# Kernel tuning notes

Measured on AMD Instinct MI355X. Metric: run time of the kernel, lower is better.

The kernel has to match this reference:

```python
import jax, jax.numpy as jnp
import numpy as np

H = 16  # n_heads

def _split_heads(x, n_heads):
    B, S, Dm = x.shape
    return x.reshape(B, S, n_heads, Dm // n_heads).transpose(0, 2, 1, 3)  # [B,H,S,D]

def _matmul_prefix_sum(x, y, z):
    """Faithful, efficient form of the TF matmul_prefix_sum.
    TF builds yz[s] = y[s] (x) z[s] outer products, cumsums over s, then
    contracts with x[t]/ (t+1).  That equals a causal-masked bilinear form:
      out[t, j] = (1/(t+1)) * sum_{s<=t} (x[t]. y[s]) * z[s, j]
    so we compute (x y^T * tril / idx) @ z without the 5D intermediate.
    """
    S = x.shape[2]
    idx = jnp.arange(1, S + 1, dtype=x.dtype)[:, None]        # position 1..S
    mask = jnp.tril(jnp.ones((S, S), dtype=x.dtype))
    scores = jnp.einsum('bhtd,bhsd->bhts', x, y) * (mask / idx)
    return jnp.einsum('bhts,bhsj->bhtj', scores, z)

def setup_inputs() -> dict:
    key = jax.random.key(0)
    ks = jax.random.split(key, 12)
    B, S, Dm = 2, 1024, 1024
    f32 = jnp.float32
    rn = lambda k, shp: jax.random.normal(k, shp, dtype=f32)
    w_scale = f32(1.0 / np.sqrt(Dm))
    return {
        'v': rn(ks[0], (B, S, Dm)),
        'k': rn(ks[1], (B, S, Dm)),
        'q': rn(ks[2], (B, S, Dm)),
        'p': rn(ks[3], (B, S, Dm)),
        'wq_k': rn(ks[4], (Dm, Dm)) * w_scale, 'wq_b': jnp.zeros((Dm,), f32),
        'wk_k': rn(ks[5], (Dm, Dm)) * w_scale, 'wk_b': jnp.zeros((Dm,), f32),
        'wv_k': rn(ks[6], (Dm, Dm)) * w_scale, 'wv_b': jnp.zeros((Dm,), f32),
        'wc_k': rn(ks[7], (Dm, Dm)) * w_scale, 'wc_b': jnp.zeros((Dm,), f32),
    }

def reference(v, k, q, p, wq_k, wq_b, wk_k, wk_b, wv_k, wv_b, wc_k, wc_b):
    B, S, Dm = q.shape
    D = Dm // H
    norm_d = 1.0 / jnp.sqrt(jnp.asarray(D, q.dtype))
    ph = _split_heads(p, H)                                    # [B,H,S,D]
    qh = _split_heads((q @ wq_k + wq_b) * norm_d, H)
    kh = _split_heads(k @ wk_k + wk_b, H)
    vh = _split_heads(v @ wv_k + wv_b, H)
    # elu(p q^T)+1 then transpose -> indexed [B,H,t(query),s(p-position)]
    attn_pack = jax.nn.elu(jnp.einsum('bhtd,bhsd->bhts', qh, ph)) + 1.0
    attn_unpack = _matmul_prefix_sum(qh, kh, attn_pack)        # [B,H,S,S]
    attn_unpack = jax.nn.softmax(attn_unpack, axis=-1)
    attn_out = _matmul_prefix_sum(attn_unpack, attn_pack, vh)  # [B,H,S,D]
    attn_out = attn_out.transpose(0, 2, 1, 3).reshape(B, S, Dm)
    return attn_out @ wc_k + wc_b
```

## Files before the change

kernel.cpp:

```cpp
#include <hip/hip_runtime.h>

#define DEVI static __device__ __forceinline__

using s16x8 = __attribute__((ext_vector_type(8))) short;
using f32x4 = __attribute__((ext_vector_type(4))) float;
using u32x4 = __attribute__((ext_vector_type(4))) unsigned int;

static constexpr int H  = 16;
static constexpr int S  = 1024;
static constexpr int DM = 1024;
static constexpr int NB = 2;
static constexpr int BS = NB * S;
static constexpr long SS  = (long)S * S;
static constexpr long HSS = (long)H * SS;
static constexpr long SDM = (long)S * DM;

DEVI unsigned short f2bf(float f) {
    union { float f; unsigned u; } c; c.f = f;
    c.u += 0x7FFFu + ((c.u >> 16) & 1u);
    return (unsigned short)(c.u >> 16);
}
DEVI float bf2f(unsigned short v) {
    union { unsigned u; float f; } c; c.u = ((unsigned)v) << 16;
    return c.f;
}

DEVI void gload16(const unsigned short* g, unsigned short* l) {
    __builtin_amdgcn_global_load_lds(
        (const __attribute__((address_space(1))) unsigned int*)g,
        (__attribute__((address_space(3))) unsigned int*)l, 16, 0, 0);
}

enum { EPI_BFB = 0, EPI_VTB, EPI_PACK, EPI_PACK2, EPI_MASK, EPI_EXP, EPI_SMASK, EPI_BF, EPI_OUT };

template<int TM, int TN, int EPI, bool CK, bool CS, bool SWZ, bool REVY>
__global__ __launch_bounds__((TM/64)*(TN/64)*64)
void gemmT(const unsigned short* __restrict__ Aall, long a_sb, long a_sh, int lda,
           const unsigned short* __restrict__ Ball, long b_sb, long b_sh, int ldb,
           void* __restrict__ Oall, void* __restrict__ O2, long o_sb, long o_sh, int ldo,
           const float* __restrict__ bias, int bstride, int K, int NV)
{
    constexpr int WN = TN / 64, WM = TM / 64, NWV = WM * WN, NTHR = NWV * 64;
    constexpr int IA = (TM * 8) / NTHR, IB = (TN * 8) / NTHR;

    int bx, by, bz;
    if (SWZ) {
        const int L = (int)blockIdx.x + ((int)blockIdx.y << 3) + ((int)blockIdx.z << 6);
        const int g = L & 7, r = L >> 3;
        bz = g + ((r >> 6) << 3);
        bx = r & 7;
        by = 7 - ((r >> 3) & 7);
    } else {
        bx = blockIdx.x;
        by = REVY ? (int)gridDim.y - 1 - (int)blockIdx.y : (int)blockIdx.y;
        bz = blockIdx.z;
    }
    const int m0 = by * TM, n0 = bx * TN;
    if (CS && n0 > m0 + TM - 1) return;
    const int zb = bz >> 4, zh = bz & 15;
    const unsigned short* Ap = Aall + (long)zb * a_sb + (long)zh * a_sh;
    const unsigned short* Bp = Ball + (long)zb * b_sb + (long)zh * b_sh;
    const float* bi = bias + (long)zh * bstride;

    __shared__ alignas(16) unsigned short lA[TM * 64];
    __shared__ alignas(16) unsigned short lB[TN * 64];

    const int tid = threadIdx.x, w = tid >> 6, lane = tid & 63;
    const int lr = lane & 15, lg = lane >> 4;
    const int wm = (w / WN) * 64, wn = (w % WN) * 64;

    const unsigned short* gA[IA]; int loA[IA];
    const unsigned short* gB[IB]; int loB[IB];
#pragma unroll
    for (int i = 0; i < IA; ++i) {
        const int q = i * NTHR + tid, row = q >> 3, slot = q & 7;
        gA[i]  = Ap + (long)(m0 + row) * lda + ((slot ^ (row & 7)) * 8);
        loA[i] = (i * NWV + w) * 512;
    }
#pragma unroll
    for (int i = 0; i < IB; ++i) {
        const int q = i * NTHR + tid, row = q >> 3, slot = q & 7;
        int rb = n0 + row; if (rb >= NV) rb = NV - 1;
        gB[i]  = Bp + (long)rb * ldb + ((slot ^ (row & 7)) * 8);
        loB[i] = (i * NWV + w) * 512;
    }

    int abase[4], axor[4], bbase[4], bxor[4];
#pragma unroll
    for (int f = 0; f < 4; ++f) {
        const int ra = wm + f * 16 + lr;
        abase[f] = ra * 64; axor[f] = (ra & 7) * 8;
        const int rb = wn + f * 16 + lr;
        bbase[f] = rb * 64; bxor[f] = (rb & 7) * 8;
    }

    f32x4 acc[4][4] = {};
    const int Keff = CK ? ((K < m0 + TM) ? K : m0 + TM) : K;

    for (int k0 = 0; k0 < Keff; k0 += 64) {
#pragma unroll
        for (int i = 0; i < IA; ++i) gload16(gA[i] + k0, &lA[loA[i]]);
#pragma unroll
        for (int i = 0; i < IB; ++i) gload16(gB[i] + k0, &lB[loB[i]]);
        __syncthreads();
#pragma unroll
        for (int kk = 0; kk < 64; kk += 32) {
            s16x8 af[4], bv[4];
#pragma unroll
            for (int f = 0; f < 4; ++f) {
                af[f] = *reinterpret_cast<const s16x8*>(&lA[abase[f] + ((kk + 8 * lg) ^ axor[f])]);
                bv[f] = *reinterpret_cast<const s16x8*>(&lB[bbase[f] + ((kk + 8 * lg) ^ bxor[f])]);
            }
#pragma unroll
            for (int fm = 0; fm < 4; ++fm)
#pragma unroll
                for (int fn = 0; fn < 4; ++fn)
                    acc[fm][fn] = __builtin_amdgcn_mfma_f32_16x16x32_bf16(af[fm], bv[fn], acc[fm][fn], 0, 0, 0);
        }
        __syncthreads();
    }

    const long obase = (long)zb * o_sb + (long)zh * o_sh;
#pragma unroll
    for (int fm = 0; fm < 4; ++fm)
#pragma unroll
        for (int fn = 0; fn < 4; ++fn) {
            const int t0 = m0 + wm + fm * 16 + lg * 4;
            const int gn = n0 + wn + fn * 16 + lr;
            if (gn >= NV) continue;
            if constexpr (EPI == EPI_PACK2) {
                ushort4 pt;
                unsigned short* o1 = (unsigned short*)Oall;
                unsigned short* o2 = (unsigned short*)O2;
#pragma unroll
                for (int r = 0; r < 4; ++r) {
                    float vv = acc[fm][fn][r];
                    vv = vv > 0.f ? vv + 1.f : __expf(vv);
                    const unsigned short b = f2bf(vv);
                    o1[obase + (long)(t0 + r) * ldo + gn] = b;
                    ((unsigned short*)&pt)[r] = b;
                }
                *reinterpret_cast<ushort4*>(&o2[obase + (long)gn * ldo + t0]) = pt;
            } else {
#pragma unroll
                for (int r = 0; r < 4; ++r) {
                    const int gm = t0 + r;
                    float vv = acc[fm][fn][r];
                    const long o = obase + (long)gm * ldo + gn;
                    if constexpr (EPI == EPI_BFB) {
                        ((unsigned short*)Oall)[o] = f2bf(vv + bi[gn]);
                    } else if constexpr (EPI == EPI_VTB) {
                        ((unsigned short*)Oall)[o] = f2bf(vv + bi[gm]);
                    } else if constexpr (EPI == EPI_PACK) {
                        vv = vv > 0.f ? vv + 1.f : __expf(vv);
                        ((unsigned short*)Oall)[o] = f2bf(vv);
                    } else if constexpr (EPI == EPI_MASK) {
                        vv = (gn <= gm) ? vv / (float)(gm + 1) : 0.f;
                        ((unsigned short*)Oall)[o] = f2bf(vv);
                    } else if constexpr (EPI == EPI_EXP) {
                        ((unsigned short*)Oall)[o] = f2bf(__expf(vv));
                    } else if constexpr (EPI == EPI_SMASK) {
                        vv = (gn <= gm) ? vv * bias[(long)bz * S + gm] / (float)(gm + 1) : 0.f;
                        ((unsigned short*)Oall)[o] = f2bf(vv);
                    } else if constexpr (EPI == EPI_BF) {
                        ((unsigned short*)Oall)[o] = f2bf(vv);
                    } else {
                        ((float*)Oall)[o] = vv + bi[gn];
                    }
                }
            }
        }
}

__global__ __launch_bounds__(256)
void rowsum_inv(const unsigned short* __restrict__ E, float* __restrict__ inv)
{
    const int w = threadIdx.x >> 6, lane = threadIdx.x & 63;
    const long row = (long)blockIdx.x * 4 + w;
    const u32x4* r4 = reinterpret_cast<const u32x4*>(E + row * S);
    u32x4 a = r4[lane * 2], b = r4[lane * 2 + 1];
    float s = 0.f;
#pragma unroll
    for (int i = 0; i < 4; ++i) {
        s += bf2f((unsigned short)(a[i] & 0xFFFF)) + bf2f((unsigned short)(a[i] >> 16));
        s += bf2f((unsigned short)(b[i] & 0xFFFF)) + bf2f((unsigned short)(b[i] >> 16));
    }
#pragma unroll
    for (int off = 32; off; off >>= 1) s += __shfl_xor(s, off);
    if (lane == 0) inv[row] = 1.f / s;
}

__global__ __launch_bounds__(256)
void cast4(const float* __restrict__ s0, const float* __restrict__ s1,
           const float* __restrict__ s2, const float* __restrict__ s3,
           unsigned short* __restrict__ dst, int n4)
{
    const int i = blockIdx.x * 256 + threadIdx.x;
    if (i >= n4) return;
    const float* s = (blockIdx.z == 0) ? s0 : (blockIdx.z == 1) ? s1 : (blockIdx.z == 2) ? s2 : s3;
    float4 x = reinterpret_cast<const float4*>(s)[i];
    ushort4 o; o.x = f2bf(x.x); o.y = f2bf(x.y); o.z = f2bf(x.z); o.w = f2bf(x.w);
    reinterpret_cast<ushort4*>(dst + (size_t)blockIdx.z * n4 * 4)[i] = o;
}

__global__ __launch_bounds__(256)
void twcast4(const float* __restrict__ s0, const float* __restrict__ s1,
             const float* __restrict__ s2, const float* __restrict__ s3,
             unsigned short* __restrict__ dstall, int n)
{
    __shared__ unsigned short t[64][72];
    const float* src = (blockIdx.z == 0) ? s0 : (blockIdx.z == 1) ? s1 : (blockIdx.z == 2) ? s2 : s3;
    const float scale = (blockIdx.z == 0) ? 0.125f : 1.0f;
    unsigned short* dst = dstall + (size_t)blockIdx.z * n * n;
    const int r0 = blockIdx.y * 64, c0 = blockIdx.x * 64;
    const int lrow = threadIdx.x >> 2, lseg = (threadIdx.x & 3) << 4;
    const float4* g4 = reinterpret_cast<const float4*>(src + (long)(r0 + lrow) * n + c0 + lseg);
    alignas(16) unsigned short tmp[16];
#pragma unroll
    for (int q = 0; q < 4; ++q) {
        float4 x = g4[q];
        tmp[4*q+0] = f2bf(x.x * scale); tmp[4*q+1] = f2bf(x.y * scale);
        tmp[4*q+2] = f2bf(x.z * scale); tmp[4*q+3] = f2bf(x.w * scale);
    }
#pragma unroll
    for (int j = 0; j < 16; ++j) t[lrow][lseg + j] = tmp[j];
    __syncthreads();
#pragma unroll
    for (int j = 0; j < 16; ++j) tmp[j] = t[lseg + j][lrow];
    unsigned short* d = dst + (long)(c0 + lrow) * n + r0 + lseg;
    *reinterpret_cast<u32x4*>(d)     = *reinterpret_cast<const u32x4*>(tmp);
    *reinterpret_cast<u32x4*>(d + 8) = *reinterpret_cast<const u32x4*>(tmp + 8);
}

__global__ __launch_bounds__(256)
void bias2(const float* __restrict__ a, const float* __restrict__ b, float* __restrict__ dst)
{
    const int i = blockIdx.x * 256 + threadIdx.x;
    if (i < DM) { dst[i] = a[i] * 0.125f; dst[DM + i] = b[i]; }
}

extern "C" void kernel_launch(void* const* d_in, const int* in_sizes, int n_in,
                              void* d_out, int out_size, void* d_ws, size_t ws_size,
                              hipStream_t stream)
{
    (void)in_sizes; (void)n_in; (void)out_size;
    const float* v_in = (const float*)d_in[0];
    const float* k_in = (const float*)d_in[1];
    const float* q_in = (const float*)d_in[2];
    const float* p_in = (const float*)d_in[3];
    const float* wq   = (const float*)d_in[4];
    const float* wqb  = (const float*)d_in[5];
    const float* wk   = (const float*)d_in[6];
    const float* wkb  = (const float*)d_in[7];
    const float* wvw  = (const float*)d_in[8];
    const float* wvb  = (const float*)d_in[9];
    const float* wc   = (const float*)d_in[10];
    const float* wcb  = (const float*)d_in[11];
    float* out = (float*)d_out;

    char* ws = (char*)d_ws;
    size_t off = 0;
    auto take = [&](size_t n) { char* p = ws + off; off += (n + 255) & ~(size_t)255; return p; };
    unsigned short* qbf = (unsigned short*)take((size_t)BS * DM * 2);
    unsigned short* kbf = (unsigned short*)take((size_t)BS * DM * 2);
    unsigned short* vbf = (unsigned short*)take((size_t)BS * DM * 2);
    unsigned short* pbf = (unsigned short*)take((size_t)BS * DM * 2);
    unsigned short* wqT = (unsigned short*)take((size_t)DM * DM * 2);
    unsigned short* wkT = (unsigned short*)take((size_t)DM * DM * 2);
    unsigned short* wvT = (unsigned short*)take((size_t)DM * DM * 2);
    unsigned short* wcT = (unsigned short*)take((size_t)DM * DM * 2);
    float*          bq2 = (float*)take((size_t)2 * DM * 4);
    float*          inv = (float*)take((size_t)NB * H * S * 4);
    unsigned short* qh  = (unsigned short*)take((size_t)BS * DM * 2);
    unsigned short* kh  = (unsigned short*)take((size_t)BS * DM * 2);
    unsigned short* vhT = (unsigned short*)take((size_t)BS * DM * 2);
    unsigned short* ao  = (unsigned short*)take((size_t)BS * DM * 2);
    const size_t ssz = (size_t)NB * HSS * 2;
    unsigned short* B1 = (unsigned short*)take(ssz);
    unsigned short* B2 = (unsigned short*)take(ssz);
    unsigned short* B3 = (unsigned short*)take(ssz);
    const bool dual = (ws_size >= off + ssz);
    unsigned short* B4 = dual ? (unsigned short*)take(ssz) : nullptr;
    (void)kbf; (void)wkT;

    const int n4 = BS * DM / 4;
    const dim3 b256(256), b128(128);

    cast4<<<dim3(n4 / 256, 1, 4), b256, 0, stream>>>(q_in, k_in, v_in, p_in, qbf, n4);
    twcast4<<<dim3(16, 16, 4), b256, 0, stream>>>(wq, wk, wvw, wc, wqT, DM);
    bias2<<<dim3(4), b256, 0, stream>>>(wqb, wkb, bq2);

    gemmT<64,128,EPI_BFB,false,false,false,false><<<dim3(8, 32, 2), b128, 0, stream>>>(
        qbf, 0, (long)BS*DM, DM,  wqT, 0, (long)DM*DM, DM,  qh, nullptr, 0, (long)BS*DM, DM,
        bq2, DM, DM, DM);
    gemmT<64,128,EPI_VTB,false,false,false,false><<<dim3(8, 16, 2), b128, 0, stream>>>(
        wvT, 0, 0, DM,  vbf, 0, SDM, DM,  vhT, nullptr, 0, (long)DM*S, S,
        wvb, 0, DM, S);

    unsigned short *sqkbuf, *ptbuf, *pbuf, *ebuf, *s2buf;
    if (dual) {
        gemmT<128,128,EPI_PACK2,false,false,true,false><<<dim3(8, 8, 32), b256, 0, stream>>>(
            qh, SDM, 64, DM,  pbf, SDM, 64, DM,  B1, B2, HSS, SS, S,  wvb, 0, 64, S);
        pbuf = B1; ptbuf = B2; sqkbuf = B3; ebuf = B4; s2buf = B3;
    } else {
        gemmT<128,128,EPI_PACK,false,false,true,false><<<dim3(8, 8, 32), b256, 0, stream>>>(
            pbf, SDM, 64, DM,  qh, SDM, 64, DM,  B1, nullptr, HSS, SS, S,  wvb, 0, 64, S);
        ptbuf = B1; sqkbuf = B2; ebuf = B3; pbuf = B1; s2buf = B2;
    }
    gemmT<128,128,EPI_MASK,false,true,true,false><<<dim3(8, 8, 32), b256, 0, stream>>>(
        qh, SDM, 64, DM,  kh, SDM, 64, DM,  sqkbuf, nullptr, HSS, SS, S,  wvb, 0, 64, S);
    gemmT<128,128,EPI_EXP,true,false,true,false><<<dim3(8, 8, 32), b256, 0, stream>>>(
        sqkbuf, HSS, SS, S,  ptbuf, HSS, SS, S,  ebuf, nullptr, HSS, SS, S,  wvb, 0, S, S);
    rowsum_inv<<<dim3(NB*H*S/4), b256, 0, stream>>>(ebuf, inv);
    if (!dual) {
        gemmT<128,128,EPI_PACK,false,false,true,false><<<dim3(8, 8, 32), b256, 0, stream>>>(
            qh, SDM, 64, DM,  pbf, SDM, 64, DM,  B1, nullptr, HSS, SS, S,  wvb, 0, 64, S);
    }
    gemmT<128,128,EPI_SMASK,false,true,true,false><<<dim3(8, 8, 32), b256, 0, stream>>>(
        ebuf, HSS, SS, S,  pbuf, HSS, SS, S,  s2buf, nullptr, HSS, SS, S,  inv, 0, S, S);
    gemmT<128,64,EPI_BF,true,false,false,true><<<dim3(1, 8, 32), b128, 0, stream>>>(
        s2buf, HSS, SS, S,  vhT, (long)DM*S, (long)64*S, S,  ao, nullptr, SDM, 64, DM,
        wvb, 0, S, 64);
    gemmT<64,128,EPI_OUT,false,false,false,false><<<dim3(8, 32, 1), b128, 0, stream>>>(
        ao, 0, 0, DM,  wcT, 0, 0, DM,  out, nullptr, 0, 0, DM,  wcb, 0, DM, DM);
}
```

Measured before the change: 307.9 us.

## Fuse softmax row sums into exp GEMM, merge pack/QK and prep kernels

The exp GEMM epilogue now accumulates per-row sums with shuffles and atomicAdd into a zeroed buffer, so the separate rowsum pass over the full S×S exp matrix is no longer needed. The SMASK epilogue divides by those sums directly. The elu-pack GEMM and the masked QK GEMM are merged into one launch, a single-k-step kernel covering both jobs. The three cast kernels are merged into one prep launch, and the global→LDS loads are interleaved. This removes a full read of a large bf16 buffer and several launches, at the cost of atomic contention and summing unrounded fp32 values instead of the stored bf16 ones.

```diff
diff --git a/kernel.cpp b/kernel.cpp
--- a/kernel.cpp
+++ b/kernel.cpp
@@ -38,10 +38,12 @@
 void gemmT(const unsigned short* __restrict__ Aall, long a_sb, long a_sh, int lda,
            const unsigned short* __restrict__ Ball, long b_sb, long b_sh, int ldb,
            void* __restrict__ Oall, void* __restrict__ O2, long o_sb, long o_sh, int ldo,
-           const float* __restrict__ bias, int bstride, int K, int NV)
+           const float* __restrict__ bias, int bstride, float* __restrict__ sums,
+           int K, int NV)
 {
     constexpr int WN = TN / 64, WM = TM / 64, NWV = WM * WN, NTHR = NWV * 64;
     constexpr int IA = (TM * 8) / NTHR, IB = (TN * 8) / NTHR;
+    constexpr int IMX = IA > IB ? IA : IB;
 
     int bx, by, bz;
     if (SWZ) {
@@ -99,9 +101,10 @@
 
     for (int k0 = 0; k0 < Keff; k0 += 64) {
 #pragma unroll
-        for (int i = 0; i < IA; ++i) gload16(gA[i] + k0, &lA[loA[i]]);
-#pragma unroll
-        for (int i = 0; i < IB; ++i) gload16(gB[i] + k0, &lB[loB[i]]);
+        for (int i = 0; i < IMX; ++i) {
+            if (i < IA) gload16(gA[i] + k0, &lA[loA[i]]);
+            if (i < IB) gload16(gB[i] + k0, &lB[loB[i]]);
+        }
         __syncthreads();
 #pragma unroll
         for (int kk = 0; kk < 64; kk += 32) {
@@ -121,122 +124,210 @@
     }
 
     const long obase = (long)zb * o_sb + (long)zh * o_sh;
+    if constexpr (EPI == EPI_EXP) {
+#pragma unroll
+        for (int fm = 0; fm < 4; ++fm) {
+            const int t0 = m0 + wm + fm * 16 + lg * 4;
+            float es[4] = {0.f, 0.f, 0.f, 0.f};
+#pragma unroll
+            for (int fn = 0; fn < 4; ++fn) {
+                const int gn = n0 + wn + fn * 16 + lr;
+#pragma unroll
+                for (int r = 0; r < 4; ++r) {
+                    const float e = __expf(acc[fm][fn][r]);
+                    ((unsigned short*)Oall)[obase + (long)(t0 + r) * ldo + gn] = f2bf(e);
+                    es[r] += e;
+                }
+            }
+#pragma unroll
+            for (int r = 0; r < 4; ++r) {
+                float s = es[r];
+                s += __shfl_xor(s, 1); s += __shfl_xor(s, 2);
+                s += __shfl_xor(s, 4); s += __shfl_xor(s, 8);
+                if (lr == 0) atomicAdd(&sums[(long)bz * S + t0 + r], s);
+            }
+        }
+    } else {
+#pragma unroll
+        for (int fm = 0; fm < 4; ++fm)
+#pragma unroll
+            for (int fn = 0; fn < 4; ++fn) {
+                const int t0 = m0 + wm + fm * 16 + lg * 4;
+                const int gn = n0 + wn + fn * 16 + lr;
+                if (gn >= NV) continue;
+                if constexpr (EPI == EPI_PACK2) {
+                    ushort4 pt;
+                    unsigned short* o1 = (unsigned short*)Oall;
+                    unsigned short* o2 = (unsigned short*)O2;
+#pragma unroll
+                    for (int r = 0; r < 4; ++r) {
+                        float vv = acc[fm][fn][r];
+                        vv = vv > 0.f ? vv + 1.f : __expf(vv);
+                        const unsigned short b = f2bf(vv);
+                        o1[obase + (long)(t0 + r) * ldo + gn] = b;
+                        ((unsigned short*)&pt)[r] = b;
+                    }
+                    *reinterpret_cast<ushort4*>(&o2[obase + (long)gn * ldo + t0]) = pt;
+                } else {
+#pragma unroll
+                    for (int r = 0; r < 4; ++r) {
+                        const int gm = t0 + r;
+                        float vv = acc[fm][fn][r];
+                        const long o = obase + (long)gm * ldo + gn;
+                        if constexpr (EPI == EPI_BFB) {
+                            ((unsigned short*)Oall)[o] = f2bf(vv + bi[gn]);
+                        } else if constexpr (EPI == EPI_VTB) {
+                            ((unsigned short*)Oall)[o] = f2bf(vv + bi[gm]);
+                        } else if constexpr (EPI == EPI_PACK) {
+                            vv = vv > 0.f ? vv + 1.f : __expf(vv);
+                            ((unsigned short*)Oall)[o] = f2bf(vv);
+                        } else if constexpr (EPI == EPI_MASK) {
+                            vv = (gn <= gm) ? vv / (float)(gm + 1) : 0.f;
+                            ((unsigned short*)Oall)[o] = f2bf(vv);
+                        } else if constexpr (EPI == EPI_SMASK) {
+                            vv = (gn <= gm)
+                               ? vv / (sums[(long)bz * S + gm] * (float)(gm + 1)) : 0.f;
+                            ((unsigned short*)Oall)[o] = f2bf(vv);
+                        } else if constexpr (EPI == EPI_BF) {
+                            ((unsigned short*)Oall)[o] = f2bf(vv);
+                        } else {
+                            ((float*)Oall)[o] = vv + bi[gn];
+                        }
+                    }
+                }
+            }
+    }
+}
+
+__global__ __launch_bounds__(256)
+void packsqk(const unsigned short* __restrict__ qh,
+             const unsigned short* __restrict__ pbf,
+             const unsigned short* __restrict__ kh,
+             unsigned short* __restrict__ P, unsigned short* __restrict__ PT,
+             unsigned short* __restrict__ SQ)
+{
+    const int L = (int)blockIdx.x + ((int)blockIdx.y << 3) + ((int)blockIdx.z << 6);
+    const int g = L & 7, r = L >> 3;
+    const int bzz = g + ((r >> 6) << 3);
+    const int bx = r & 7, by = 7 - ((r >> 3) & 7);
+    const int job = bzz >> 5, zz = bzz & 31;
+    const int m0 = by * 128, n0 = bx * 128;
+    if (job && n0 > m0 + 127) return;
+    const int zb = zz >> 4, zh = zz & 15;
+    const unsigned short* Ap = qh + (long)zb * SDM + zh * 64;
+    const unsigned short* Bp = (job ? kh : pbf) + (long)zb * SDM + zh * 64;
+
+    __shared__ alignas(16) unsigned short lA[128 * 64];
+    __shared__ alignas(16) unsigned short lB[128 * 64];
+
+    const int tid = threadIdx.x, w = tid >> 6, lane = tid & 63;
+    const int lr = lane & 15, lg = lane >> 4;
+    const int wm = (w >> 1) << 6, wn = (w & 1) << 6;
+
+#pragma unroll
+    for (int i = 0; i < 4; ++i) {
+        const int q = i * 256 + tid, row = q >> 3, slot = q & 7;
+        const int gs = (slot ^ (row & 7)) * 8;
+        gload16(Ap + (long)(m0 + row) * DM + gs, &lA[(i * 4 + w) * 512]);
+        gload16(Bp + (long)(n0 + row) * DM + gs, &lB[(i * 4 + w) * 512]);
+    }
+    __syncthreads();
+
+    f32x4 acc[4][4] = {};
+#pragma unroll
+    for (int kk = 0; kk < 64; kk += 32) {
+        s16x8 af[4], bv[4];
+#pragma unroll
+        for (int f = 0; f < 4; ++f) {
+            const int ra = wm + f * 16 + lr;
+            af[f] = *reinterpret_cast<const s16x8*>(&lA[ra * 64 + ((kk + 8 * lg) ^ ((ra & 7) * 8))]);
+            const int rb = wn + f * 16 + lr;
+            bv[f] = *reinterpret_cast<const s16x8*>(&lB[rb * 64 + ((kk + 8 * lg) ^ ((rb & 7) * 8))]);
+        }
+#pragma unroll
+        for (int fm = 0; fm < 4; ++fm)
+#pragma unroll
+            for (int fn = 0; fn < 4; ++fn)
+                acc[fm][fn] = __builtin_amdgcn_mfma_f32_16x16x32_bf16(af[fm], bv[fn], acc[fm][fn], 0, 0, 0);
+    }
+
+    const long obase = (long)zz * SS;
 #pragma unroll
     for (int fm = 0; fm < 4; ++fm)
 #pragma unroll
         for (int fn = 0; fn < 4; ++fn) {
             const int t0 = m0 + wm + fm * 16 + lg * 4;
             const int gn = n0 + wn + fn * 16 + lr;
-            if (gn >= NV) continue;
-            if constexpr (EPI == EPI_PACK2) {
+            if (job == 0) {
                 ushort4 pt;
-                unsigned short* o1 = (unsigned short*)Oall;
-                unsigned short* o2 = (unsigned short*)O2;
-#pragma unroll
-                for (int r = 0; r < 4; ++r) {
-                    float vv = acc[fm][fn][r];
+#pragma unroll
+                for (int rr = 0; rr < 4; ++rr) {
+                    float vv = acc[fm][fn][rr];
                     vv = vv > 0.f ? vv + 1.f : __expf(vv);
                     const unsigned short b = f2bf(vv);
-                    o1[obase + (long)(t0 + r) * ldo + gn] = b;
-                    ((unsigned short*)&pt)[r] = b;
+                    P[obase + (long)(t0 + rr) * S + gn] = b;
+                    ((unsigned short*)&pt)[rr] = b;
                 }
-                *reinterpret_cast<ushort4*>(&o2[obase + (long)gn * ldo + t0]) = pt;
+                *reinterpret_cast<ushort4*>(&PT[obase + (long)gn * S + t0]) = pt;
             } else {
 #pragma unroll
-                for (int r = 0; r < 4; ++r) {
-                    const int gm = t0 + r;
-                    float vv = acc[fm][fn][r];
-                    const long o = obase + (long)gm * ldo + gn;
-                    if constexpr (EPI == EPI_BFB) {
-                        ((unsigned short*)Oall)[o] = f2bf(vv + bi[gn]);
-                    } else if constexpr (EPI == EPI_VTB) {
-                        ((unsigned short*)Oall)[o] = f2bf(vv + bi[gm]);
-                    } else if constexpr (EPI == EPI_PACK) {
-                        vv = vv > 0.f ? vv + 1.f : __expf(vv);
-                        ((unsigned short*)Oall)[o] = f2bf(vv);
-                    } else if constexpr (EPI == EPI_MASK) {
-                        vv = (gn <= gm) ? vv / (float)(gm + 1) : 0.f;
-                        ((unsigned short*)Oall)[o] = f2bf(vv);
-                    } else if constexpr (EPI == EPI_EXP) {
-                        ((unsigned short*)Oall)[o] = f2bf(__expf(vv));
-                    } else if constexpr (EPI == EPI_SMASK) {
-                        vv = (gn <= gm) ? vv * bias[(long)bz * S + gm] / (float)(gm + 1) : 0.f;
-                        ((unsigned short*)Oall)[o] = f2bf(vv);
-                    } else if constexpr (EPI == EPI_BF) {
-                        ((unsigned short*)Oall)[o] = f2bf(vv);
-                    } else {
-                        ((float*)Oall)[o] = vv + bi[gn];
-                    }
+                for (int rr = 0; rr < 4; ++rr) {
+                    const int gm = t0 + rr;
+                    float vv = acc[fm][fn][rr];
+                    vv = (gn <= gm) ? vv / (float)(gm + 1) : 0.f;
+                    SQ[obase + (long)gm * S + gn] = f2bf(vv);
                 }
             }
         }
 }
 
 __global__ __launch_bounds__(256)
-void rowsum_inv(const unsigned short* __restrict__ E, float* __restrict__ inv)
+void prep(const float* __restrict__ q_in, const float* __restrict__ k_in,
+          const float* __restrict__ v_in, const float* __restrict__ p_in,
+          const float* __restrict__ wq, const float* __restrict__ wk,
+          const float* __restrict__ wv, const float* __restrict__ wc,
+          const float* __restrict__ wqb, const float* __restrict__ wkb,
+          unsigned short* __restrict__ qbf, unsigned short* __restrict__ wqT,
+          float* __restrict__ bq2, int n4)
 {
-    const int w = threadIdx.x >> 6, lane = threadIdx.x & 63;
-    const long row = (long)blockIdx.x * 4 + w;
-    const u32x4* r4 = reinterpret_cast<const u32x4*>(E + row * S);
-    u32x4 a = r4[lane * 2], b = r4[lane * 2 + 1];
-    float s = 0.f;
-#pragma unroll
-    for (int i = 0; i < 4; ++i) {
-        s += bf2f((unsigned short)(a[i] & 0xFFFF)) + bf2f((unsigned short)(a[i] >> 16));
-        s += bf2f((unsigned short)(b[i] & 0xFFFF)) + bf2f((unsigned short)(b[i] >> 16));
-    }
-#pragma unroll
-    for (int off = 32; off; off >>= 1) s += __shfl_xor(s, off);
-    if (lane == 0) inv[row] = 1.f / s;
-}
-
-__global__ __launch_bounds__(256)
-void cast4(const float* __restrict__ s0, const float* __restrict__ s1,
-           const float* __restrict__ s2, const float* __restrict__ s3,
-           unsigned short* __restrict__ dst, int n4)
-{
-    const int i = blockIdx.x * 256 + threadIdx.x;
-    if (i >= n4) return;
-    const float* s = (blockIdx.z == 0) ? s0 : (blockIdx.z == 1) ? s1 : (blockIdx.z == 2) ? s2 : s3;
-    float4 x = reinterpret_cast<const float4*>(s)[i];
-    ushort4 o; o.x = f2bf(x.x); o.y = f2bf(x.y); o.z = f2bf(x.z); o.w = f2bf(x.w);
-    reinterpret_cast<ushort4*>(dst + (size_t)blockIdx.z * n4 * 4)[i] = o;
-}
-
-__global__ __launch_bounds__(256)
-void twcast4(const float* __restrict__ s0, const float* __restrict__ s1,
-             const float* __restrict__ s2, const float* __restrict__ s3,
-             unsigned short* __restrict__ dstall, int n)
-{
-    __shared__ unsigned short t[64][72];
-    const float* src = (blockIdx.z == 0) ? s0 : (blockIdx.z == 1) ? s1 : (blockIdx.z == 2) ? s2 : s3;
-    const float scale = (blockIdx.z == 0) ? 0.125f : 1.0f;
-    unsigned short* dst = dstall + (size_t)blockIdx.z * n * n;
-    const int r0 = blockIdx.y * 64, c0 = blockIdx.x * 64;
-    const int lrow = threadIdx.x >> 2, lseg = (threadIdx.x & 3) << 4;
-    const float4* g4 = reinterpret_cast<const float4*>(src + (long)(r0 + lrow) * n + c0 + lseg);
-    alignas(16) unsigned short tmp[16];
-#pragma unroll
-    for (int q = 0; q < 4; ++q) {
-        float4 x = g4[q];
-        tmp[4*q+0] = f2bf(x.x * scale); tmp[4*q+1] = f2bf(x.y * scale);
-        tmp[4*q+2] = f2bf(x.z * scale); tmp[4*q+3] = f2bf(x.w * scale);
-    }
-#pragma unroll
-    for (int j = 0; j < 16; ++j) t[lrow][lseg + j] = tmp[j];
-    __syncthreads();
-#pragma unroll
-    for (int j = 0; j < 16; ++j) tmp[j] = t[lseg + j][lrow];
-    unsigned short* d = dst + (long)(c0 + lrow) * n + r0 + lseg;
-    *reinterpret_cast<u32x4*>(d)     = *reinterpret_cast<const u32x4*>(tmp);
-    *reinterpret_cast<u32x4*>(d + 8) = *reinterpret_cast<const u32x4*>(tmp + 8);
-}
-
-__global__ __launch_bounds__(256)
-void bias2(const float* __restrict__ a, const float* __restrict__ b, float* __restrict__ dst)
-{
-    const int i = blockIdx.x * 256 + threadIdx.x;
-    if (i < DM) { dst[i] = a[i] * 0.125f; dst[DM + i] = b[i]; }
+    const int z = blockIdx.z, bx = blockIdx.x, tid = threadIdx.x;
+    if (z < 4) {
+        const int i = bx * 256 + tid;
+        if (i >= n4) return;
+        const float* s = (z == 0) ? q_in : (z == 1) ? k_in : (z == 2) ? v_in : p_in;
+        float4 x = reinterpret_cast<const float4*>(s)[i];
+        ushort4 o; o.x = f2bf(x.x); o.y = f2bf(x.y); o.z = f2bf(x.z); o.w = f2bf(x.w);
+        reinterpret_cast<ushort4*>(qbf + (size_t)z * n4 * 4)[i] = o;
+    } else if (z < 8) {
+        if (bx >= 256) return;
+        __shared__ unsigned short t[64][72];
+        const int zz = z - 4;
+        const float* src = (zz == 0) ? wq : (zz == 1) ? wk : (zz == 2) ? wv : wc;
+        const float scale = (zz == 0) ? 0.125f : 1.0f;
+        unsigned short* dst = wqT + (size_t)zz * DM * DM;
+        const int r0 = (bx >> 4) * 64, c0 = (bx & 15) * 64;
+        const int lrow = tid >> 2, lseg = (tid & 3) << 4;
+        const float4* g4 = reinterpret_cast<const float4*>(src + (long)(r0 + lrow) * DM + c0 + lseg);
+        alignas(16) unsigned short tmp[16];
+#pragma unroll
+        for (int qq = 0; qq < 4; ++qq) {
+            float4 x = g4[qq];
+            tmp[4*qq+0] = f2bf(x.x * scale); tmp[4*qq+1] = f2bf(x.y * scale);
+            tmp[4*qq+2] = f2bf(x.z * scale); tmp[4*qq+3] = f2bf(x.w * scale);
+        }
+#pragma unroll
+        for (int j = 0; j < 16; ++j) t[lrow][lseg + j] = tmp[j];
+        __syncthreads();
+#pragma unroll
+        for (int j = 0; j < 16; ++j) tmp[j] = t[lseg + j][lrow];
+        unsigned short* d = dst + (long)(c0 + lrow) * DM + r0 + lseg;
+        *reinterpret_cast<u32x4*>(d)     = *reinterpret_cast<const u32x4*>(tmp);
+        *reinterpret_cast<u32x4*>(d + 8) = *reinterpret_cast<const u32x4*>(tmp + 8);
+    } else {
+        if (bx >= 4) return;
+        const int i = bx * 256 + tid;
+        if (i < DM) { bq2[i] = wqb[i] * 0.125f; bq2[DM + i] = wkb[i]; }
+    }
 }
 
 extern "C" void kernel_launch(void* const* d_in, const int* in_sizes, int n_in,
@@ -270,7 +361,7 @@
     unsigned short* wvT = (unsigned short*)take((size_t)DM * DM * 2);
     unsigned short* wcT = (unsigned short*)take((size_t)DM * DM * 2);
     float*          bq2 = (float*)take((size_t)2 * DM * 4);
-    float*          inv = (float*)take((size_t)NB * H * S * 4);
+    float*          sums= (float*)take((size_t)NB * H * S * 4);
     unsigned short* qh  = (unsigned short*)take((size_t)BS * DM * 2);
     unsigned short* kh  = (unsigned short*)take((size_t)BS * DM * 2);
     unsigned short* vhT = (unsigned short*)take((size_t)BS * DM * 2);
@@ -286,41 +377,41 @@
     const int n4 = BS * DM / 4;
     const dim3 b256(256), b128(128);
 
-    cast4<<<dim3(n4 / 256, 1, 4), b256, 0, stream>>>(q_in, k_in, v_in, p_in, qbf, n4);
-    twcast4<<<dim3(16, 16, 4), b256, 0, stream>>>(wq, wk, wvw, wc, wqT, DM);
-    bias2<<<dim3(4), b256, 0, stream>>>(wqb, wkb, bq2);
+    hipMemsetAsync(sums, 0, (size_t)NB * H * S * 4, stream);
+    prep<<<dim3(n4 / 256, 1, 9), b256, 0, stream>>>(
+        q_in, k_in, v_in, p_in, wq, wk, wvw, wc, wqb, wkb, qbf, wqT, bq2, n4);
 
     gemmT<64,128,EPI_BFB,false,false,false,false><<<dim3(8, 32, 2), b128, 0, stream>>>(
         qbf, 0, (long)BS*DM, DM,  wqT, 0, (long)DM*DM, DM,  qh, nullptr, 0, (long)BS*DM, DM,
-        bq2, DM, DM, DM);
+        bq2, DM, nullptr, DM, DM);
     gemmT<64,128,EPI_VTB,false,false,false,false><<<dim3(8, 16, 2), b128, 0, stream>>>(
         wvT, 0, 0, DM,  vbf, 0, SDM, DM,  vhT, nullptr, 0, (long)DM*S, S,
-        wvb, 0, DM, S);
-
-    unsigned short *sqkbuf, *ptbuf, *pbuf, *ebuf, *s2buf;
+        wvb, 0, nullptr, DM, S);
+
+    unsigned short *ptbuf, *pbuf, *ebuf, *s2buf, *sqkbuf;
     if (dual) {
-        gemmT<128,128,EPI_PACK2,false,false,true,false><<<dim3(8, 8, 32), b256, 0, stream>>>(
-            qh, SDM, 64, DM,  pbf, SDM, 64, DM,  B1, B2, HSS, SS, S,  wvb, 0, 64, S);
+        packsqk<<<dim3(8, 8, 64), b256, 0, stream>>>(qh, pbf, kh, B1, B2, B3);
         pbuf = B1; ptbuf = B2; sqkbuf = B3; ebuf = B4; s2buf = B3;
     } else {
         gemmT<128,128,EPI_PACK,false,false,true,false><<<dim3(8, 8, 32), b256, 0, stream>>>(
-            pbf, SDM, 64, DM,  qh, SDM, 64, DM,  B1, nullptr, HSS, SS, S,  wvb, 0, 64, S);
+            pbf, SDM, 64, DM,  qh, SDM, 64, DM,  B1, nullptr, HSS, SS, S,  wvb, 0, nullptr, 64, S);
         ptbuf = B1; sqkbuf = B2; ebuf = B3; pbuf = B1; s2buf = B2;
-    }
-    gemmT<128,128,EPI_MASK,false,true,true,false><<<dim3(8, 8, 32), b256, 0, stream>>>(
-        qh, SDM, 64, DM,  kh, SDM, 64, DM,  sqkbuf, nullptr, HSS, SS, S,  wvb, 0, 64, S);
+        gemmT<128,128,EPI_MASK,false,true,true,false><<<dim3(8, 8, 32), b256, 0, stream>>>(
+            qh, SDM, 64, DM,  kh, SDM, 64, DM,  sqkbuf, nullptr, HSS, SS, S,  wvb, 0, nullptr, 64, S);
+    }
     gemmT<128,128,EPI_EXP,true,false,true,false><<<dim3(8, 8, 32), b256, 0, stream>>>(
-        sqkbuf, HSS, SS, S,  ptbuf, HSS, SS, S,  ebuf, nullptr, HSS, SS, S,  wvb, 0, S, S);
-    rowsum_inv<<<dim3(NB*H*S/4), b256, 0, stream>>>(ebuf, inv);
+        sqkbuf, HSS, SS, S,  ptbuf, HSS, SS, S,  ebuf, nullptr, HSS, SS, S,
+        wvb, 0, sums, S, S);
     if (!dual) {
         gemmT<128,128,EPI_PACK,false,false,true,false><<<dim3(8, 8, 32), b256, 0, stream>>>(
-            qh, SDM, 64, DM,  pbf, SDM, 64, DM,  B1, nullptr, HSS, SS, S,  wvb, 0, 64, S);
+            qh, SDM, 64, DM,  pbf, SDM, 64, DM,  B1, nullptr, HSS, SS, S,  wvb, 0, nullptr, 64, S);
     }
     gemmT<128,128,EPI_SMASK,false,true,true,false><<<dim3(8, 8, 32), b256, 0, stream>>>(
-        ebuf, HSS, SS, S,  pbuf, HSS, SS, S,  s2buf, nullptr, HSS, SS, S,  inv, 0, S, S);
+        ebuf, HSS, SS, S,  pbuf, HSS, SS, S,  s2buf, nullptr, HSS, SS, S,
+        nullptr, 0, sums, S, S);
     gemmT<128,64,EPI_BF,true,false,false,true><<<dim3(1, 8, 32), b128, 0, stream>>>(
         s2buf, HSS, SS, S,  vhT, (long)DM*S, (long)64*S, S,  ao, nullptr, SDM, 64, DM,
-        wvb, 0, S, 64);
+        wvb, 0, nullptr, S, 64);
     gemmT<64,128,EPI_OUT,false,false,false,false><<<dim3(8, 32, 1), b128, 0, stream>>>(
-        ao, 0, 0, DM,  wcT, 0, 0, DM,  out, nullptr, 0, 0, DM,  wcb, 0, DM, DM);
-}
+        ao, 0, 0, DM,  wcT, 0, 0, DM,  out, nullptr, 0, 0, DM,  wcb, 0, nullptr, DM, DM);
+}
```

New measurement: 311.0 us. No clear change (+1.0%).
